# Performance work log

Hardware: AMD Instinct MI355X
Metric: run time of the kernel (lower is better)

## Reference

```python
import jax, jax.numpy as jnp
from jax import lax
import numpy as np
import math

# --- static config (matches init_kwargs) ---
B, L, C_IN = 64, 1024, 16
D, H, D_FF = 256, 8, 1024
HS, E_LAYERS, OUT = 256, 2, 1
MA, FACTOR = 25, 3
TOP_K = int(FACTOR * math.log(L))  # 20


def _ln(x, g, b, eps=1e-5):
    m = x.mean(-1, keepdims=True)
    v = ((x - m) ** 2).mean(-1, keepdims=True)
    return (x - m) / jnp.sqrt(v + eps) * g + b


def _series_decomp(x, k):
    # x: [B, L, C]; replicate-pad then moving average (AvgPool1d stride 1)
    pad = (k - 1) // 2
    front = jnp.repeat(x[:, :1, :], pad, axis=1)
    end = jnp.repeat(x[:, -1:, :], pad, axis=1)
    xp = jnp.concatenate([front, x, end], axis=1)  # [B, L+k-1, C]
    cs = jnp.cumsum(xp, axis=1)
    cs = jnp.concatenate([jnp.zeros_like(cs[:, :1]), cs], axis=1)
    mm = (cs[:, k:] - cs[:, :-k]) / k  # [B, L, C]
    return x - mm, mm


def _autocorrelation(q, k, v):
    # q,k,v: [B, L, H, E] -> eval-mode Autoformer AutoCorrelation
    Bq, Lq, Hq, Eq = q.shape
    qf = jnp.fft.rfft(q.transpose(0, 2, 3, 1), axis=-1)  # [B,H,E,F]
    kf = jnp.fft.rfft(k.transpose(0, 2, 3, 1), axis=-1)
    corr = jnp.fft.irfft(qf * jnp.conj(kf), n=Lq, axis=-1)  # [B,H,E,L]
    mean_value = corr.mean(axis=(1, 2))  # [B, L]
    weights, delay = lax.top_k(mean_value, TOP_K)  # [B, K]
    tmp_corr = jax.nn.softmax(weights, axis=-1)
    vals = v.transpose(0, 2, 3, 1)  # [B,H,E,L]
    init = jnp.arange(Lq)

    def step(acc, dw):
        d, w = dw  # d: [B] int, w: [B] float
        idx = (init[None, :] + d[:, None]) % Lq  # circular delayed gather == roll
        pat = jnp.take_along_axis(vals, idx[:, None, None, :], axis=-1)
        return acc + pat * w[:, None, None, None], None

    agg, _ = lax.scan(step, jnp.zeros_like(vals), (delay.T, tmp_corr.T))
    return agg.transpose(0, 3, 1, 2)  # [B, L, H, E]


def _forward(x_enc, conv1_w, conv1_b, conv2_w, conv2_b, cnn_ln_g, cnn_ln_b,
             proj_w, proj_b, proj_ln_g, proj_ln_b,
             Wq, bq, Wk, bk, Wv, bv, Wo, bo, Wff1, Wff2,
             rp1_w, rp1_b, rp_ln_g, rp_ln_b, rp2_w, rp2_b):
    Bb = x_enc.shape[0]
    dn = ('NCH', 'OIH', 'NCH')
    # CNN frontend (dropout = identity in eval)
    h = lax.conv_general_dilated(x_enc.transpose(0, 2, 1), conv1_w, (1,), [(1, 1)],
                                 dimension_numbers=dn) + conv1_b[None, :, None]
    h = jax.nn.relu(h)
    h = lax.conv_general_dilated(h, conv2_w, (1,), [(1, 1)],
                                 dimension_numbers=dn) + conv2_b[None, :, None]
    h = jax.nn.relu(h)
    enc = _ln(h.transpose(0, 2, 1), cnn_ln_g, cnn_ln_b)  # [B, L, D]

    pooled_parts = []
    for i in range(E_LAYERS):
        q = (enc @ Wq[i] + bq[i]).reshape(Bb, L, H, D // H)
        k = (enc @ Wk[i] + bk[i]).reshape(Bb, L, H, D // H)
        v = (enc @ Wv[i] + bv[i]).reshape(Bb, L, H, D // H)
        ac = _autocorrelation(q, k, v).reshape(Bb, L, D)
        new_x = ac @ Wo[i] + bo[i]
        x = enc + new_x
        x, _ = _series_decomp(x, MA)
        y = jax.nn.gelu(jnp.einsum('bld,fd->blf', x, Wff1[i]), approximate=False)
        y = jnp.einsum('blf,df->bld', y, Wff2[i])
        enc, _ = _series_decomp(x + y, MA)
        pooled_parts.append(enc[:, -1, :])

    pooled = jnp.concatenate(pooled_parts, axis=-1)  # [B, e_layers*D]
    input_embed = _ln(jax.nn.relu(x_enc.reshape(Bb, -1) @ proj_w + proj_b),
                      proj_ln_g, proj_ln_b)  # [B, HS]
    final = jnp.concatenate([pooled, input_embed], axis=-1)
    o = jax.nn.relu(final @ rp1_w + rp1_b)
    o = _ln(o, rp_ln_g, rp_ln_b)
    o = o @ rp2_w + rp2_b  # [B, 1]
    return o.squeeze(-1)


def setup_inputs() -> dict:
    key = jax.random.key(0)
    ks = iter(jax.random.split(key, 32))

    def nrm(shape, s=0.02):
        return jax.random.normal(next(ks), shape, jnp.float32) * s

    inp = {
        'x_enc': jax.random.normal(next(ks), (B, L, C_IN), jnp.float32),
        'conv1_w': nrm((D, C_IN, 3), 0.1), 'conv1_b': jnp.zeros((D,), jnp.float32),
        'conv2_w': nrm((D, D, 3), 0.05), 'conv2_b': jnp.zeros((D,), jnp.float32),
        'cnn_ln_g': jnp.ones((D,), jnp.float32), 'cnn_ln_b': jnp.zeros((D,), jnp.float32),
        'proj_w': nrm((L * C_IN, HS)), 'proj_b': jnp.zeros((HS,), jnp.float32),
        'proj_ln_g': jnp.ones((HS,), jnp.float32), 'proj_ln_b': jnp.zeros((HS,), jnp.float32),
        'Wq': nrm((E_LAYERS, D, D)), 'bq': jnp.zeros((E_LAYERS, D), jnp.float32),
        'Wk': nrm((E_LAYERS, D, D)), 'bk': jnp.zeros((E_LAYERS, D), jnp.float32),
        'Wv': nrm((E_LAYERS, D, D)), 'bv': jnp.zeros((E_LAYERS, D), jnp.float32),
        'Wo': nrm((E_LAYERS, D, D)), 'bo': jnp.zeros((E_LAYERS, D), jnp.float32),
        'Wff1': nrm((E_LAYERS, D_FF, D)),
        'Wff2': nrm((E_LAYERS, D, D_FF)),
        'rp1_w': nrm((E_LAYERS * D + HS, HS)), 'rp1_b': jnp.zeros((HS,), jnp.float32),
        'rp_ln_g': jnp.ones((HS,), jnp.float32), 'rp_ln_b': jnp.zeros((HS,), jnp.float32),
        'rp2_w': nrm((HS, OUT)), 'rp2_b': jnp.zeros((OUT,), jnp.float32),
    }
    return inp


def reference(x_enc, conv1_w, conv1_b, conv2_w, conv2_b, cnn_ln_g, cnn_ln_b,
              proj_w, proj_b, proj_ln_g, proj_ln_b,
              Wq, bq, Wk, bk, Wv, bv, Wo, bo, Wff1, Wff2,
              rp1_w, rp1_b, rp_ln_g, rp_ln_b, rp2_w, rp2_b):
    return _forward(x_enc, conv1_w, conv1_b, conv2_w, conv2_b, cnn_ln_g, cnn_ln_b,
                    proj_w, proj_b, proj_ln_g, proj_ln_b,
                    Wq, bq, Wk, bk, Wv, bv, Wo, bo, Wff1, Wff2,
                    rp1_w, rp1_b, rp_ln_g, rp_ln_b, rp2_w, rp2_b)
```

## Files before the change

### kernel.cpp

```cpp
#include <hip/hip_runtime.h>
#include <math.h>

#define FLAG_ACC     1
#define FLAG_RELU    2
#define FLAG_GELU    4
#define FLAG_ABF16   8
#define FLAG_OBF16  16
#define FLAG_RESB16 32

typedef __attribute__((ext_vector_type(8))) short short8;
typedef __attribute__((ext_vector_type(4))) short short4v;
typedef __attribute__((ext_vector_type(4))) float f32x4;

__device__ __forceinline__ short f2bf(float f) {
  unsigned u = __builtin_bit_cast(unsigned, f);
  unsigned r = u + 0x7fffu + ((u >> 16) & 1u);
  return (short)(r >> 16);
}
__device__ __forceinline__ float bf2f(short s) {
  unsigned u = ((unsigned)(unsigned short)s) << 16;
  return __builtin_bit_cast(float, u);
}
__device__ __forceinline__ void load_lds16(const void* g, void* lds) {
  __builtin_amdgcn_global_load_lds(
      (const __attribute__((address_space(1))) void*)g,
      (__attribute__((address_space(3))) void*)lds, 16, 0, 0);
}

__global__ __launch_bounds__(256) void gemm_f32(
    const float* __restrict__ A, const float* __restrict__ B, float* __restrict__ C,
    int M, int N, int K, int a_shift,
    const float* __restrict__ bias, const float* __restrict__ residual, int flags)
{
  __shared__ float As[16][65];
  __shared__ float Bs[16][64];
  const int tid = threadIdx.x;
  const int tx = tid & 15, ty = tid >> 4;
  const int row0 = blockIdx.y * 64;
  const int col0 = blockIdx.x * 64;
  int kbeg = 0, kend = K;
  if ((int)gridDim.z > 1) {
    int kchunk = ((K + (int)gridDim.z - 1) / (int)gridDim.z + 15) & ~15;
    kbeg = (int)blockIdx.z * kchunk;
    kend = min(K, kbeg + kchunk);
  }
  float acc[4][4] = {};
  const int a_m = tid >> 2;
  const int a_k = (tid & 3) << 2;
  const int b_n = (tid & 15) << 2;
  const int b_k = tid >> 4;
  for (int k0 = kbeg; k0 < kend; k0 += 16) {
    int srow = row0 + a_m + a_shift;
    float4 av = make_float4(0.f, 0.f, 0.f, 0.f);
    if (srow >= 0 && srow < M)
      av = *reinterpret_cast<const float4*>(A + (long long)srow * K + (k0 + a_k));
    As[a_k + 0][a_m] = av.x; As[a_k + 1][a_m] = av.y;
    As[a_k + 2][a_m] = av.z; As[a_k + 3][a_m] = av.w;
    float4 bv = make_float4(0.f, 0.f, 0.f, 0.f);
    int brow = k0 + b_k;
    if (brow < K)
      bv = *reinterpret_cast<const float4*>(B + (long long)brow * N + (col0 + b_n));
    Bs[b_k][b_n + 0] = bv.x; Bs[b_k][b_n + 1] = bv.y;
    Bs[b_k][b_n + 2] = bv.z; Bs[b_k][b_n + 3] = bv.w;
    __syncthreads();
#pragma unroll
    for (int kk = 0; kk < 16; kk++) {
      float ar[4], br[4];
#pragma unroll
      for (int i = 0; i < 4; i++) ar[i] = As[kk][ty * 4 + i];
#pragma unroll
      for (int j = 0; j < 4; j++) br[j] = Bs[kk][tx * 4 + j];
#pragma unroll
      for (int i = 0; i < 4; i++)
#pragma unroll
        for (int j = 0; j < 4; j++)
          acc[i][j] += ar[i] * br[j];
    }
    __syncthreads();
  }
  if ((int)gridDim.z > 1) {
#pragma unroll
    for (int i = 0; i < 4; i++) {
      int r = row0 + ty * 4 + i; if (r >= M) continue;
#pragma unroll
      for (int j = 0; j < 4; j++) {
        int c = col0 + tx * 4 + j; if (c >= N) continue;
        atomicAdd(&C[(long long)r * N + c], acc[i][j]);
      }
    }
    return;
  }
#pragma unroll
  for (int i = 0; i < 4; i++) {
    int r = row0 + ty * 4 + i; if (r >= M) continue;
#pragma unroll
    for (int j = 0; j < 4; j++) {
      int c = col0 + tx * 4 + j; if (c >= N) continue;
      float v = acc[i][j];
      if (bias)     v += bias[c];
      if (residual) v += residual[(long long)r * N + c];
      if (flags & FLAG_ACC)  v += C[(long long)r * N + c];
      if (flags & FLAG_RELU) v = fmaxf(v, 0.f);
      if (flags & FLAG_GELU) v = 0.5f * v * (1.f + erff(v * 0.70710678118654752f));
      C[(long long)r * N + c] = v;
    }
  }
}

__global__ __launch_bounds__(512) void gemm_bt8(
    const void* __restrict__ Av, const short* __restrict__ Btb, void* __restrict__ Cv,
    const float* __restrict__ residual, const float* __restrict__ bias,
    int M, int N, int K, int lda, int flags, int tapped)
{
  __shared__ __align__(16) short Asl[8192];
  __shared__ __align__(16) short Bsl[8192];
  const int tid = threadIdx.x;
  const int row0 = blockIdx.x * 128;
  const int col0 = blockIdx.y * 128;
  const int lane = tid & 63;
  const int wave = tid >> 6;
  const int wm = (wave >> 1) * 32;
  const int wn = (wave & 1) * 64;
  const int fm = lane & 15;
  const int k8c = lane >> 4;
  const int mr = tid >> 2;
  const int mkc = tid & 3;
  const int msw = mr & 7;
  const bool a_dma = (flags & FLAG_ABF16) && !tapped;

  f32x4 acc[2][4] = {};
  for (int k0 = 0; k0 < K; k0 += 64) {
    __syncthreads();
#pragma unroll
    for (int u = 0; u < 2; u++) {
      int p = (wave * 2 + u) * 64 + lane;
      int r = p >> 3;
      int kc = (p & 7) ^ (r & 7);
      load_lds16(Btb + (long long)(col0 + r) * K + k0 + kc * 8,
                 (char*)Bsl + (wave * 2 + u) * 1024);
    }
    if (a_dma) {
      const short* Ab = (const short*)Av;
#pragma unroll
      for (int u = 0; u < 2; u++) {
        int p = (wave * 2 + u) * 64 + lane;
        int r = p >> 3;
        int kc = (p & 7) ^ (r & 7);
        load_lds16(Ab + (long long)(row0 + r) * lda + k0 + kc * 8,
                   (char*)Asl + (wave * 2 + u) * 1024);
      }
    } else {
      int arow = row0 + mr + (tapped ? (k0 >> 8) - 1 : 0);
      int acol = tapped ? (k0 & 255) : k0;
      bool ok = (arow >= 0 && arow < M);
      if (flags & FLAG_ABF16) {
        const short* ga = (const short*)Av + (long long)arow * lda + acol + mkc * 16;
        short8 z;
#pragma unroll
        for (int u = 0; u < 8; u++) z[u] = 0;
#pragma unroll
        for (int j = 0; j < 2; j++) {
          short8 v = ok ? *(const short8*)(ga + j * 8) : z;
          *(short8*)&Asl[(mr * 8 + ((mkc * 2 + j) ^ msw)) * 8] = v;
        }
      } else {
        const float* ga = (const float*)Av + (long long)arow * lda + acol + mkc * 16;
#pragma unroll
        for (int j = 0; j < 2; j++) {
          float4 f0 = make_float4(0.f,0.f,0.f,0.f), f1 = f0;
          if (ok) { f0 = *(const float4*)(ga + j * 8); f1 = *(const float4*)(ga + j * 8 + 4); }
          short8 v;
          v[0]=f2bf(f0.x); v[1]=f2bf(f0.y); v[2]=f2bf(f0.z); v[3]=f2bf(f0.w);
          v[4]=f2bf(f1.x); v[5]=f2bf(f1.y); v[6]=f2bf(f1.z); v[7]=f2bf(f1.w);
          *(short8*)&Asl[(mr * 8 + ((mkc * 2 + j) ^ msw)) * 8] = v;
        }
      }
    }
    __syncthreads();
#pragma unroll
    for (int kk8 = 0; kk8 < 8; kk8 += 4) {
      short8 af[2], bf[4];
#pragma unroll
      for (int i = 0; i < 2; i++) {
        int r = wm + i * 16 + fm;
        af[i] = *(short8*)&Asl[(r * 8 + ((kk8 + k8c) ^ (r & 7))) * 8];
      }
#pragma unroll
      for (int j = 0; j < 4; j++) {
        int r = wn + j * 16 + fm;
        bf[j] = *(short8*)&Bsl[(r * 8 + ((kk8 + k8c) ^ (r & 7))) * 8];
      }
#pragma unroll
      for (int i = 0; i < 2; i++)
#pragma unroll
        for (int j = 0; j < 4; j++)
          acc[i][j] = __builtin_amdgcn_mfma_f32_16x16x32_bf16(af[i], bf[j], acc[i][j], 0, 0, 0);
    }
  }
#pragma unroll
  for (int i = 0; i < 2; i++) {
    const int mbase = row0 + wm + i * 16 + (lane >> 4) * 4;
#pragma unroll
    for (int j = 0; j < 4; j++) {
      const int n = col0 + wn + j * 16 + fm;
      const float bs = bias ? bias[n] : 0.f;
#pragma unroll
      for (int r = 0; r < 4; r++) {
        long long idx = (long long)(mbase + r) * N + n;
        float v = acc[i][j][r] + bs;
        if (residual) {
          if (flags & FLAG_RESB16) v += bf2f(((const short*)residual)[idx]);
          else                     v += residual[idx];
        }
        if (flags & FLAG_ACC)  v += ((const float*)Cv)[idx];
        if (flags & FLAG_RELU) v = fmaxf(v, 0.f);
        if (flags & FLAG_GELU) v = 0.5f * v * (1.f + erff(v * 0.70710678118654752f));
        if (flags & FLAG_OBF16) ((short*)Cv)[idx] = f2bf(v);
        else                    ((float*)Cv)[idx] = v;
      }
    }
  }
}

__global__ __launch_bounds__(512) void gemm_qkT(
    const short* __restrict__ Ab, const short* __restrict__ Bth,
    const short* __restrict__ Btl, float* __restrict__ QT,
    const float* __restrict__ bias, int K)
{
  __shared__ __align__(16) char smem[24576];
  short* Asl = (short*)smem;
  short* Bhi = (short*)(smem + 8192);
  short* Blo = (short*)(smem + 16384);
  const int tid = threadIdx.x;
  const int row0 = blockIdx.x * 128;
  const int col0 = blockIdx.y * 128;
  const int lane = tid & 63;
  const int wave = tid >> 6;
  const int wm = (wave >> 1) * 32;
  const int wn = (wave & 1) * 64;
  const int fm = lane & 15;
  const int k8c = lane >> 4;

  f32x4 acc[2][4] = {};
  for (int k0 = 0; k0 < K; k0 += 32) {
    __syncthreads();
    {
      int p = wave * 64 + lane;
      int r = p >> 2;
      int kc = (p & 3) ^ ((r >> 1) & 3);
      long long ao = (long long)(row0 + r) * 256 + k0 + kc * 8;
      long long go = (long long)(col0 + r) * K + k0 + kc * 8;
      int lo = wave * 1024;
      load_lds16(Ab + ao, (char*)Asl + lo);
      load_lds16(Bth + go, (char*)Bhi + lo);
      load_lds16(Btl + go, (char*)Blo + lo);
    }
    __syncthreads();
    short8 af[2], bh[4], bl[4];
#pragma unroll
    for (int i = 0; i < 2; i++) {
      int r = wm + i * 16 + fm;
      af[i] = *(short8*)&Asl[(r * 4 + (k8c ^ ((r >> 1) & 3))) * 8];
    }
#pragma unroll
    for (int j = 0; j < 4; j++) {
      int r = wn + j * 16 + fm;
      int p = (r * 4 + (k8c ^ ((r >> 1) & 3))) * 8;
      bh[j] = *(short8*)&Bhi[p];
      bl[j] = *(short8*)&Blo[p];
    }
#pragma unroll
    for (int i = 0; i < 2; i++)
#pragma unroll
      for (int j = 0; j < 4; j++) {
        acc[i][j] = __builtin_amdgcn_mfma_f32_16x16x32_bf16(af[i], bh[j], acc[i][j], 0, 0, 0);
        acc[i][j] = __builtin_amdgcn_mfma_f32_16x16x32_bf16(af[i], bl[j], acc[i][j], 0, 0, 0);
      }
  }
#pragma unroll
  for (int i = 0; i < 2; i++) {
    const int mbase = row0 + wm + i * 16 + (lane >> 4) * 4;
    const int bb = mbase >> 10;
    const int l  = mbase & 1023;
#pragma unroll
    for (int j = 0; j < 4; j++) {
      const int n = col0 + wn + j * 16 + fm;
      const float bs = bias[n];
      float4 o = make_float4(acc[i][j][0] + bs, acc[i][j][1] + bs,
                             acc[i][j][2] + bs, acc[i][j][3] + bs);
      *(float4*)&QT[((long long)(bb * 512 + n) << 10) + l] = o;
    }
  }
}

#define SKW(i) ((i) + ((i) >> 5))

__device__ __forceinline__ int rev4_10(int f) {
  return ((f & 3) << 8) | (((f >> 2) & 3) << 6) | (((f >> 4) & 3) << 4)
       | (((f >> 6) & 3) << 2) | ((f >> 8) & 3);
}

template<int M, bool INV, int NCH>
__device__ __forceinline__ void fft_stageN(float2 (*__restrict__ buf)[1056],
                                           const float2* __restrict__ tw, int t) {
  constexpr int LOG2M = (M == 256) ? 8 : (M == 64) ? 6 : (M == 16) ? 4 : (M == 4) ? 2 : 0;
  const int j = t & (M - 1);
  const int base = ((t >> LOG2M) << (LOG2M + 2)) | j;
  float2 w = tw[SKW(j << (8 - LOG2M))];
  const float c1 = w.x, s1 = INV ? -w.y : w.y;
  const float c2 = c1 * c1 - s1 * s1, s2 = 2.f * c1 * s1;
  const float c3 = c2 * c1 - s2 * s1, s3 = c2 * s1 + s2 * c1;
#pragma unroll
  for (int ch = 0; ch < NCH; ch++) {
    float2* s = buf[ch];
    float2 a0 = s[SKW(base)];
    float2 b0 = s[SKW(base + M)];
    float2 d0 = s[SKW(base + 2 * M)];
    float2 e0 = s[SKW(base + 3 * M)];
    float t0r = a0.x + d0.x, t0i = a0.y + d0.y;
    float t1r = a0.x - d0.x, t1i = a0.y - d0.y;
    float t2r = b0.x + e0.x, t2i = b0.y + e0.y;
    float t3r = b0.x - e0.x, t3i = b0.y - e0.y;
    float y0r = t0r + t2r, y0i = t0i + t2i;
    float y2r = t0r - t2r, y2i = t0i - t2i;
    float y1r, y1i, y3r, y3i;
    if (!INV) { y1r = t1r + t3i; y1i = t1i - t3r; y3r = t1r - t3i; y3i = t1i + t3r; }
    else      { y1r = t1r - t3i; y1i = t1i + t3r; y3r = t1r + t3i; y3i = t1i - t3r; }
    s[SKW(base)]         = make_float2(y0r, y0i);
    s[SKW(base + M)]     = make_float2(y1r * c1 - y1i * s1, y1r * s1 + y1i * c1);
    s[SKW(base + 2 * M)] = make_float2(y2r * c2 - y2i * s2, y2r * s2 + y2i * c2);
    s[SKW(base + 3 * M)] = make_float2(y3r * c3 - y3i * s3, y3r * s3 + y3i * c3);
  }
}

__global__ __launch_bounds__(256) void fft_cross(
    const float* __restrict__ QT, float* __restrict__ Rpart)
{
  __shared__ float2 buf[4][1056];
  __shared__ float2 tw[264];
  const int tid = threadIdx.x;
  const int b = blockIdx.x & 63;
  const int g = blockIdx.x >> 6;
  {
    float s, c;
    sincosf(-1.5707963267948966f * (float)tid * (1.f / 256.f), &s, &c);
    tw[SKW(tid)] = make_float2(c, s);
  }
  const float* Qb = QT + (long long)b * 524288;
  const int c0 = g * 16;
  float4 qv[4], kv[4];
#pragma unroll
  for (int c = 0; c < 4; c++) {
    qv[c] = *(const float4*)(Qb + ((long long)(c0 + c) << 10) + tid * 4);
    kv[c] = *(const float4*)(Qb + ((long long)(256 + c0 + c) << 10) + tid * 4);
  }
  float aR[4] = {0.f, 0.f, 0.f, 0.f}, aI[4] = {0.f, 0.f, 0.f, 0.f};
  __syncthreads();
  for (int q4 = 0; q4 < 4; q4++) {
    const int i0 = tid * 4;
#pragma unroll
    for (int c = 0; c < 4; c++) {
      buf[c][SKW(i0 + 0)] = make_float2(qv[c].x, kv[c].x);
      buf[c][SKW(i0 + 1)] = make_float2(qv[c].y, kv[c].y);
      buf[c][SKW(i0 + 2)] = make_float2(qv[c].z, kv[c].z);
      buf[c][SKW(i0 + 3)] = make_float2(qv[c].w, kv[c].w);
    }
    if (q4 < 3) {
      const int cb = c0 + (q4 + 1) * 4;
#pragma unroll
      for (int c = 0; c < 4; c++) {
        qv[c] = *(const float4*)(Qb + ((long long)(cb + c) << 10) + tid * 4);
        kv[c] = *(const float4*)(Qb + ((long long)(256 + cb + c) << 10) + tid * 4);
      }
    }
    __syncthreads();
    fft_stageN<256, false, 4>(buf, tw, tid); __syncthreads();
    fft_stageN<64,  false, 4>(buf, tw, tid); __syncthreads();
    fft_stageN<16,  false, 4>(buf, tw, tid); __syncthreads();
    fft_stageN<4,   false, 4>(buf, tw, tid); __syncthreads();
    fft_stageN<1,   false, 4>(buf, tw, tid); __syncthreads();
#pragma unroll
    for (int u = 0; u < 4; u++) {
      const int f = tid + (u << 8);
      const int p1 = SKW(rev4_10(f));
      const int p2 = SKW(rev4_10((1024 - f) & 1023));
#pragma unroll
      for (int c = 0; c < 4; c++) {
        float2 z1 = buf[c][p1];
        float2 z2 = buf[c][p2];
        float Qr = 0.5f * (z1.x + z2.x), Qi = 0.5f * (z1.y - z2.y);
        float Kr = 0.5f * (z1.y + z2.y), Ki = 0.5f * (z2.x - z1.x);
        aR[u] += Qr * Kr + Qi * Ki;
        aI[u] += Qi * Kr - Qr * Ki;
      }
    }
    __syncthreads();
  }
  float* Rp = Rpart + (long long)(g * 64 + b) * 2048;
#pragma unroll
  for (int u = 0; u < 4; u++) {
    Rp[tid + (u << 8)] = aR[u];
    Rp[1024 + tid + (u << 8)] = aI[u];
  }
}

__global__ __launch_bounds__(256) void fft_inv(
    const float* __restrict__ Rpart, float* __restrict__ MV)
{
  __shared__ float2 ping[1056], tw[264];
  const int tid = threadIdx.x;
  const int b = blockIdx.x;
  {
    float s, c;
    sincosf(-1.5707963267948966f * (float)tid * (1.f / 256.f), &s, &c);
    tw[SKW(tid)] = make_float2(c, s);
  }
#pragma unroll
  for (int u = 0; u < 4; u++) {
    int f = tid + (u << 8);
    float sr = 0.f, si = 0.f;
#pragma unroll
    for (int g = 0; g < 16; g++) {
      const float* Rp = Rpart + (long long)(g * 64 + b) * 2048;
      sr += Rp[f];
      si += Rp[1024 + f];
    }
    ping[SKW(f)] = make_float2(sr, si);
  }
  __syncthreads();
  float2 (*bp)[1056] = reinterpret_cast<float2 (*)[1056]>(ping);
  fft_stageN<256, true, 1>(bp, tw, tid); __syncthreads();
  fft_stageN<64,  true, 1>(bp, tw, tid); __syncthreads();
  fft_stageN<16,  true, 1>(bp, tw, tid); __syncthreads();
  fft_stageN<4,   true, 1>(bp, tw, tid); __syncthreads();
  fft_stageN<1,   true, 1>(bp, tw, tid); __syncthreads();
  const float sc = 1.f / (1024.f * 256.f);
#pragma unroll
  for (int u = 0; u < 4; u++) {
    int p = tid + (u << 8);
    MV[(long long)b * 1024 + rev4_10(p)] = ping[SKW(p)].x * sc;
  }
}

__global__ void prep_weights(
    const float* __restrict__ conv2_w, const float* __restrict__ Wq,
    const float* __restrict__ Wk, const float* __restrict__ Wff1,
    const float* __restrict__ Wff2,
    const float* __restrict__ bq, const float* __restrict__ bk,
    short* __restrict__ CB2Tb, short* __restrict__ QKTH, short* __restrict__ QKTL,
    short* __restrict__ WFF1b, short* __restrict__ WFF2b, float* __restrict__ BQK)
{
  const int total = 196608 + 262144 + 524288 + 524288 + 1024;
  for (int idx = blockIdx.x * 256 + threadIdx.x; idx < total;
       idx += gridDim.x * 256) {
    int t = idx;
    if (t < 196608) {
      int o = t / 768, rem = t % 768, kk = rem >> 8, i = rem & 255;
      CB2Tb[t] = f2bf(conv2_w[(o * 256 + i) * 3 + kk]);
    } else if ((t -= 196608) < 262144) {
      int L = t >> 17, rem = t & 131071, r = rem >> 8, k = rem & 255;
      float val = (r < 256) ? Wq[L * 65536 + k * 256 + r]
                            : Wk[L * 65536 + k * 256 + (r - 256)];
      short h = f2bf(val);
      QKTH[t] = h;
      QKTL[t] = f2bf(val - bf2f(h));
    } else if ((t -= 262144) < 524288) {
      WFF1b[t] = f2bf(Wff1[t]);
    } else if ((t -= 524288) < 524288) {
      WFF2b[t] = f2bf(Wff2[t]);
    } else {
      t -= 524288;
      int L = t >> 9, j = t & 511;
      BQK[t] = (j < 256) ? bq[L * 256 + j] : bk[L * 256 + (j - 256)];
    }
  }
}

__global__ void vo_finish(const float* __restrict__ WVO, const float* __restrict__ Wo,
                          const float* __restrict__ bv, const float* __restrict__ bo,
                          short* __restrict__ WVOTb, float* __restrict__ BVO)
{
  const int total = 131072 + 512;
  for (int idx = blockIdx.x * 256 + threadIdx.x; idx < total;
       idx += gridDim.x * 256) {
    if (idx < 131072) {
      int L = idx >> 16, rem = idx & 65535, n = rem >> 8, k = rem & 255;
      WVOTb[idx] = f2bf(WVO[L * 65536 + k * 256 + n]);
    } else {
      int j = idx - 131072;
      int L = j >> 8, n = j & 255;
      float acc = bo[L * 256 + n];
      for (int k = 0; k < 256; k++)
        acc += bv[L * 256 + k] * Wo[(long long)L * 65536 + k * 256 + n];
      BVO[j] = acc;
    }
  }
}

__global__ __launch_bounds__(256) void conv1_direct(
    const float* __restrict__ x, const float* __restrict__ w,
    const float* __restrict__ bias, short* __restrict__ out)
{
  __shared__ float xs[66][16];
  const int b = blockIdx.y, lg = blockIdx.x, tid = threadIdx.x;
  const int l0 = lg * 64;
  for (int idx = tid; idx < 1056; idx += 256) {
    int r = idx >> 4, c = idx & 15;
    int l = l0 + r - 1;
    xs[r][c] = (l >= 0 && l < 1024) ? x[((long long)b * 1024 + l) * 16 + c] : 0.f;
  }
  float wr[48];
#pragma unroll
  for (int u = 0; u < 48; u++) wr[u] = w[tid * 48 + u];
  const float bs = bias[tid];
  __syncthreads();
  for (int r = 0; r < 64; r++) {
    float acc = bs;
#pragma unroll
    for (int i = 0; i < 16; i++) {
      acc += xs[r + 0][i] * wr[i * 3 + 0];
      acc += xs[r + 1][i] * wr[i * 3 + 1];
      acc += xs[r + 2][i] * wr[i * 3 + 2];
    }
    out[((long long)b * 1024 + l0 + r) * 256 + tid] = f2bf(fmaxf(acc, 0.f));
  }
}

__global__ __launch_bounds__(256) void fixup_conv_b(
    short* __restrict__ h, const short* __restrict__ src,
    const short* __restrict__ w2b, const float* __restrict__ bias)
{
  __shared__ __align__(16) short srows[512];
  const int b = blockIdx.x >> 1;
  const int edge = blockIdx.x & 1;
  const int l = edge ? 1023 : 0;
  const int o = threadIdx.x;
  const int t0 = edge ? 1022 : 0;
  const int kk0 = edge ? 0 : 1;
  if (threadIdx.x < 64) {
    int rr = threadIdx.x >> 5, cc = threadIdx.x & 31;
    ((short8*)srows)[rr * 32 + cc] =
        ((const short8*)(src + ((long long)b * 1024 + t0 + rr) * 256))[cc];
  }
  __syncthreads();
  float acc = bias[o];
  const short* w0 = w2b + o * 768 + kk0 * 256;
  const short* w1 = w0 + 256;
#pragma unroll
  for (int c8 = 0; c8 < 32; c8++) {
    short8 wv0 = *(const short8*)(w0 + c8 * 8);
    short8 wv1 = *(const short8*)(w1 + c8 * 8);
    short8 x0 = ((short8*)srows)[c8];
    short8 x1 = ((short8*)srows)[32 + c8];
#pragma unroll
    for (int j = 0; j < 8; j++)
      acc += bf2f(x0[j]) * bf2f(wv0[j]) + bf2f(x1[j]) * bf2f(wv1[j]);
  }
  h[((long long)b * 1024 + l) * 256 + o] = f2bf(fmaxf(acc, 0.f));
}

__global__ __launch_bounds__(256) void ln_rows4(
    const float* __restrict__ in, float* __restrict__ out,
    const float* __restrict__ g, const float* __restrict__ b,
    int prerelu, int out_stride, int out_off)
{
  const int row = blockIdx.x * 4 + (threadIdx.x >> 6);
  const int lane = threadIdx.x & 63;
  float4 x = ((const float4*)(in + (long long)row * 256))[lane];
  if (prerelu) {
    x.x = fmaxf(x.x, 0.f); x.y = fmaxf(x.y, 0.f);
    x.z = fmaxf(x.z, 0.f); x.w = fmaxf(x.w, 0.f);
  }
  float s = x.x + x.y + x.z + x.w;
#pragma unroll
  for (int o = 32; o > 0; o >>= 1) s += __shfl_xor(s, o, 64);
  float mean = s * (1.f / 256.f);
  float4 d = make_float4(x.x - mean, x.y - mean, x.z - mean, x.w - mean);
  float s2 = d.x * d.x + d.y * d.y + d.z * d.z + d.w * d.w;
#pragma unroll
  for (int o = 32; o > 0; o >>= 1) s2 += __shfl_xor(s2, o, 64);
  float rsd = rsqrtf(s2 * (1.f / 256.f) + 1e-5f);
  float4 gg = ((const float4*)g)[lane];
  float4 bb = ((const float4*)b)[lane];
  float4 o4 = make_float4(d.x * rsd * gg.x + bb.x, d.y * rsd * gg.y + bb.y,
                          d.z * rsd * gg.z + bb.z, d.w * rsd * gg.w + bb.w);
  ((float4*)(out + (long long)row * out_stride + out_off))[lane] = o4;
}

__global__ __launch_bounds__(256) void ln_rows4bb(
    const short* __restrict__ in, short* __restrict__ out,
    const float* __restrict__ g, const float* __restrict__ b)
{
  const int row = blockIdx.x * 4 + (threadIdx.x >> 6);
  const int lane = threadIdx.x & 63;
  short4v xb = ((const short4v*)in)[(long long)row * 64 + lane];
  float4 x = make_float4(bf2f(xb[0]), bf2f(xb[1]), bf2f(xb[2]), bf2f(xb[3]));
  float s = x.x + x.y + x.z + x.w;
#pragma unroll
  for (int o = 32; o > 0; o >>= 1) s += __shfl_xor(s, o, 64);
  float mean = s * (1.f / 256.f);
  float4 d = make_float4(x.x - mean, x.y - mean, x.z - mean, x.w - mean);
  float s2 = d.x * d.x + d.y * d.y + d.z * d.z + d.w * d.w;
#pragma unroll
  for (int o = 32; o > 0; o >>= 1) s2 += __shfl_xor(s2, o, 64);
  float rsd = rsqrtf(s2 * (1.f / 256.f) + 1e-5f);
  float4 gg = ((const float4*)g)[lane];
  float4 bb = ((const float4*)b)[lane];
  short4v o4;
  o4[0] = f2bf(d.x * rsd * gg.x + bb.x);
  o4[1] = f2bf(d.y * rsd * gg.y + bb.y);
  o4[2] = f2bf(d.z * rsd * gg.z + bb.z);
  o4[3] = f2bf(d.w * rsd * gg.w + bb.w);
  ((short4v*)out)[(long long)row * 64 + lane] = o4;
}

__global__ void decomp4bf(const short* __restrict__ in, short* __restrict__ out,
                          float* __restrict__ fin, int finoff)
{
  const int id = blockIdx.x;
  const int c = id & 7;
  const int s = id >> 3;
  const int b = c + 8 * (s >> 8);
  const int lg = s & 255;
  const int l = lg * 4 + (threadIdx.x >> 6);
  const int c4 = threadIdx.x & 63;
  const short4v* base = (const short4v*)(in + (long long)b * 262144);
  float4 acc = make_float4(0.f, 0.f, 0.f, 0.f);
#pragma unroll
  for (int j = -12; j <= 12; j++) {
    int t = l + j;
    t = t < 0 ? 0 : (t > 1023 ? 1023 : t);
    short4v x = base[t * 64 + c4];
    acc.x += bf2f(x[0]); acc.y += bf2f(x[1]);
    acc.z += bf2f(x[2]); acc.w += bf2f(x[3]);
  }
  short4v x0 = base[l * 64 + c4];
  float4 o = make_float4(bf2f(x0[0]) - acc.x * (1.f / 25.f),
                         bf2f(x0[1]) - acc.y * (1.f / 25.f),
                         bf2f(x0[2]) - acc.z * (1.f / 25.f),
                         bf2f(x0[3]) - acc.w * (1.f / 25.f));
  short4v ob;
  ob[0] = f2bf(o.x); ob[1] = f2bf(o.y); ob[2] = f2bf(o.z); ob[3] = f2bf(o.w);
  ((short4v*)out)[((long long)b * 1024 + l) * 64 + c4] = ob;
  if (l == 1023) {
    float* f = fin + (long long)b * 768 + finoff + c4 * 4;
    f[0] = o.x; f[1] = o.y; f[2] = o.z; f[3] = o.w;
  }
}

__global__ void decomp4b(const short* __restrict__ in, short* __restrict__ out)
{
  const int id = blockIdx.x;
  const int c = id & 7;
  const int s = id >> 3;
  const int b = c + 8 * (s >> 8);
  const int lg = s & 255;
  const int l = lg * 4 + (threadIdx.x >> 6);
  const int c4 = threadIdx.x & 63;
  const short4v* base = (const short4v*)(in + (long long)b * 262144);
  float4 acc = make_float4(0.f, 0.f, 0.f, 0.f);
#pragma unroll
  for (int j = -12; j <= 12; j++) {
    int t = l + j;
    t = t < 0 ? 0 : (t > 1023 ? 1023 : t);
    short4v x = base[t * 64 + c4];
    acc.x += bf2f(x[0]); acc.y += bf2f(x[1]);
    acc.z += bf2f(x[2]); acc.w += bf2f(x[3]);
  }
  short4v x0 = base[l * 64 + c4];
  short4v o;
  o[0] = f2bf(bf2f(x0[0]) - acc.x * (1.f / 25.f));
  o[1] = f2bf(bf2f(x0[1]) - acc.y * (1.f / 25.f));
  o[2] = f2bf(bf2f(x0[2]) - acc.z * (1.f / 25.f));
  o[3] = f2bf(bf2f(x0[3]) - acc.w * (1.f / 25.f));
  ((short4v*)(out + (long long)b * 262144))[l * 64 + c4] = o;
}

__global__ __launch_bounds__(64) void topk_softmax_wave(
    const float* __restrict__ mv, float* __restrict__ wts, int* __restrict__ dly)
{
  const int b = blockIdx.x, lane = threadIdx.x;
  float v[16];
#pragma unroll
  for (int j = 0; j < 16; j++)
    v[j] = mv[(long long)b * 1024 + lane + 64 * j];
  float selv = 0.f; int seli = 0;
  for (int it = 0; it < 20; it++) {
    float bv = -1e30f; int bi = 0x7fffffff;
#pragma unroll
    for (int j = 0; j < 16; j++) {
      float x = v[j]; int idx = lane + 64 * j;
      if (x > bv || (x == bv && idx < bi)) { bv = x; bi = idx; }
    }
#pragma unroll
    for (int off = 32; off > 0; off >>= 1) {
      float ov = __shfl_xor(bv, off, 64);
      int   oi = __shfl_xor(bi, off, 64);
      if (ov > bv || (ov == bv && oi < bi)) { bv = ov; bi = oi; }
    }
    if (lane == it) { selv = bv; seli = bi; }
    if ((bi & 63) == lane) v[bi >> 6] = -1e30f;
  }
  const float w0 = __shfl(selv, 0, 64);
  float e = (lane < 20) ? __expf(selv - w0) : 0.f;
  float s = e;
#pragma unroll
  for (int off = 32; off > 0; off >>= 1) s += __shfl_xor(s, off, 64);
  if (lane < 20) {
    wts[b * 20 + lane] = e / s;
    dly[b * 20 + lane] = seli;
  }
}

__global__ void agg4b(const short* __restrict__ enc, const float* __restrict__ wts,
                      const int* __restrict__ dly, short* __restrict__ out)
{
  const int id = blockIdx.x;
  const int c = id & 7;
  const int s = id >> 3;
  const int b = c + 8 * (s >> 8);
  const int lg = s & 255;
  const int l = lg * 4 + (threadIdx.x >> 6);
  const int c4 = threadIdx.x & 63;
  const short4v* vb = (const short4v*)(enc + (long long)b * 262144);
  float4 acc = make_float4(0.f, 0.f, 0.f, 0.f);
  for (int kk = 0; kk < 20; kk++) {
    int d = dly[b * 20 + kk];
    float w = wts[b * 20 + kk];
    short4v x = vb[((l + d) & 1023) * 64 + c4];
    acc.x += w * bf2f(x[0]); acc.y += w * bf2f(x[1]);
    acc.z += w * bf2f(x[2]); acc.w += w * bf2f(x[3]);
  }
  short4v o;
  o[0] = f2bf(acc.x); o[1] = f2bf(acc.y); o[2] = f2bf(acc.z); o[3] = f2bf(acc.w);
  ((short4v*)(out + (long long)b * 262144))[l * 64 + c4] = o;
}

__global__ void init_bias(float* __restrict__ C, const float* __restrict__ bias)
{
  C[(long long)blockIdx.x * 256 + threadIdx.x] = bias[threadIdx.x];
}

__global__ void rp2_kernel(const float* __restrict__ x, const float* __restrict__ w,
// ... 148 lines not shown
```

Before: 1.278 ms.

## Stage QK GEMM epilogue through LDS and split FFT buffers into planar arrays

The QK projection epilogue now transposes its accumulator tile through shared memory in four column chunks, so each thread writes contiguous 32-byte runs of the transposed QT output instead of scattered float4 stores. Separately, the FFT kernels switch from interleaved float2 shared buffers to split real and imaginary float arrays, with matching split twiddle tables. The planar layout is meant to reduce LDS bank conflicts in the radix-4 stages. The epilogue adds extra barriers and reuses the GEMM shared memory, which assumes that region is large enough.

Result: slower. 1.331 ms (+4.1%).

```diff
diff --git a/kernel.cpp b/kernel.cpp
--- a/kernel.cpp
+++ b/kernel.cpp
@@ -277,19 +277,35 @@
         acc[i][j] = __builtin_amdgcn_mfma_f32_16x16x32_bf16(af[i], bl[j], acc[i][j], 0, 0, 0);
       }
   }
-#pragma unroll
-  for (int i = 0; i < 2; i++) {
-    const int mbase = row0 + wm + i * 16 + (lane >> 4) * 4;
-    const int bb = mbase >> 10;
-    const int l  = mbase & 1023;
-#pragma unroll
-    for (int j = 0; j < 4; j++) {
-      const int n = col0 + wn + j * 16 + fm;
-      const float bs = bias[n];
-      float4 o = make_float4(acc[i][j][0] + bs, acc[i][j][1] + bs,
-                             acc[i][j][2] + bs, acc[i][j][3] + bs);
-      *(float4*)&QT[((long long)(bb * 512 + n) << 10) + l] = o;
-    }
+  float* Tt = (float*)smem;
+  const int bb = row0 >> 10;
+  const int lbase = row0 & 1023;
+#pragma unroll
+  for (int ch = 0; ch < 4; ch++) {
+    __syncthreads();
+    int rel = ch * 32 - wn;
+    if (rel >= 0 && rel < 64) {
+      int j0 = rel >> 4;
+#pragma unroll
+      for (int jj = 0; jj < 2; jj++) {
+        int j = j0 + jj;
+        int nl = j * 16 + fm - rel;
+        float bs = bias[col0 + wn + j * 16 + fm];
+#pragma unroll
+        for (int i = 0; i < 2; i++) {
+          int l = wm + i * 16 + (lane >> 4) * 4;
+          *(float4*)&Tt[nl * 132 + l] = make_float4(
+              acc[i][j][0] + bs, acc[i][j][1] + bs,
+              acc[i][j][2] + bs, acc[i][j][3] + bs);
+        }
+      }
+    }
+    __syncthreads();
+    int col = tid >> 4;
+    int l0 = (tid & 15) * 8;
+    long long base = (((long long)(bb * 512 + col0 + ch * 32 + col)) << 10) + lbase + l0;
+    *(float4*)&QT[base]     = *(float4*)&Tt[col * 132 + l0];
+    *(float4*)&QT[base + 4] = *(float4*)&Tt[col * 132 + l0 + 4];
   }
 }
 
@@ -301,50 +317,54 @@
 }
 
 template<int M, bool INV, int NCH>
-__device__ __forceinline__ void fft_stageN(float2 (*__restrict__ buf)[1056],
-                                           const float2* __restrict__ tw, int t) {
+__device__ __forceinline__ void fft_stageS(float (*__restrict__ re)[1056],
+                                           float (*__restrict__ im)[1056],
+                                           const float* __restrict__ twc,
+                                           const float* __restrict__ tws, int t) {
   constexpr int LOG2M = (M == 256) ? 8 : (M == 64) ? 6 : (M == 16) ? 4 : (M == 4) ? 2 : 0;
   const int j = t & (M - 1);
   const int base = ((t >> LOG2M) << (LOG2M + 2)) | j;
-  float2 w = tw[SKW(j << (8 - LOG2M))];
-  const float c1 = w.x, s1 = INV ? -w.y : w.y;
+  const int ti = SKW(j << (8 - LOG2M));
+  const float c1 = twc[ti];
+  const float s1 = INV ? -tws[ti] : tws[ti];
   const float c2 = c1 * c1 - s1 * s1, s2 = 2.f * c1 * s1;
   const float c3 = c2 * c1 - s2 * s1, s3 = c2 * s1 + s2 * c1;
+  const int p0 = SKW(base), p1 = SKW(base + M), p2 = SKW(base + 2 * M), p3 = SKW(base + 3 * M);
 #pragma unroll
   for (int ch = 0; ch < NCH; ch++) {
-    float2* s = buf[ch];
-    float2 a0 = s[SKW(base)];
-    float2 b0 = s[SKW(base + M)];
-    float2 d0 = s[SKW(base + 2 * M)];
-    float2 e0 = s[SKW(base + 3 * M)];
-    float t0r = a0.x + d0.x, t0i = a0.y + d0.y;
-    float t1r = a0.x - d0.x, t1i = a0.y - d0.y;
-    float t2r = b0.x + e0.x, t2i = b0.y + e0.y;
-    float t3r = b0.x - e0.x, t3i = b0.y - e0.y;
+    float a0r = re[ch][p0], a0i = im[ch][p0];
+    float b0r = re[ch][p1], b0i = im[ch][p1];
+    float d0r = re[ch][p2], d0i = im[ch][p2];
+    float e0r = re[ch][p3], e0i = im[ch][p3];
+    float t0r = a0r + d0r, t0i = a0i + d0i;
+    float t1r = a0r - d0r, t1i = a0i - d0i;
+    float t2r = b0r + e0r, t2i = b0i + e0i;
+    float t3r = b0r - e0r, t3i = b0i - e0i;
     float y0r = t0r + t2r, y0i = t0i + t2i;
     float y2r = t0r - t2r, y2i = t0i - t2i;
     float y1r, y1i, y3r, y3i;
     if (!INV) { y1r = t1r + t3i; y1i = t1i - t3r; y3r = t1r - t3i; y3i = t1i + t3r; }
     else      { y1r = t1r - t3i; y1i = t1i + t3r; y3r = t1r + t3i; y3i = t1i - t3r; }
-    s[SKW(base)]         = make_float2(y0r, y0i);
-    s[SKW(base + M)]     = make_float2(y1r * c1 - y1i * s1, y1r * s1 + y1i * c1);
-    s[SKW(base + 2 * M)] = make_float2(y2r * c2 - y2i * s2, y2r * s2 + y2i * c2);
-    s[SKW(base + 3 * M)] = make_float2(y3r * c3 - y3i * s3, y3r * s3 + y3i * c3);
+    re[ch][p0] = y0r;                       im[ch][p0] = y0i;
+    re[ch][p1] = y1r * c1 - y1i * s1;       im[ch][p1] = y1r * s1 + y1i * c1;
+    re[ch][p2] = y2r * c2 - y2i * s2;       im[ch][p2] = y2r * s2 + y2i * c2;
+    re[ch][p3] = y3r * c3 - y3i * s3;       im[ch][p3] = y3r * s3 + y3i * c3;
   }
 }
 
 __global__ __launch_bounds__(256) void fft_cross(
     const float* __restrict__ QT, float* __restrict__ Rpart)
 {
-  __shared__ float2 buf[4][1056];
-  __shared__ float2 tw[264];
+  __shared__ float bre[4][1056], bim[4][1056];
+  __shared__ float twc[264], tws[264];
   const int tid = threadIdx.x;
   const int b = blockIdx.x & 63;
   const int g = blockIdx.x >> 6;
   {
     float s, c;
     sincosf(-1.5707963267948966f * (float)tid * (1.f / 256.f), &s, &c);
-    tw[SKW(tid)] = make_float2(c, s);
+    twc[SKW(tid)] = c;
+    tws[SKW(tid)] = s;
   }
   const float* Qb = QT + (long long)b * 524288;
   const int c0 = g * 16;
@@ -360,10 +380,10 @@
     const int i0 = tid * 4;
 #pragma unroll
     for (int c = 0; c < 4; c++) {
-      buf[c][SKW(i0 + 0)] = make_float2(qv[c].x, kv[c].x);
-      buf[c][SKW(i0 + 1)] = make_float2(qv[c].y, kv[c].y);
-      buf[c][SKW(i0 + 2)] = make_float2(qv[c].z, kv[c].z);
-      buf[c][SKW(i0 + 3)] = make_float2(qv[c].w, kv[c].w);
+      bre[c][SKW(i0 + 0)] = qv[c].x;  bim[c][SKW(i0 + 0)] = kv[c].x;
+      bre[c][SKW(i0 + 1)] = qv[c].y;  bim[c][SKW(i0 + 1)] = kv[c].y;
+      bre[c][SKW(i0 + 2)] = qv[c].z;  bim[c][SKW(i0 + 2)] = kv[c].z;
+      bre[c][SKW(i0 + 3)] = qv[c].w;  bim[c][SKW(i0 + 3)] = kv[c].w;
     }
     if (q4 < 3) {
       const int cb = c0 + (q4 + 1) * 4;
@@ -374,11 +394,11 @@
       }
     }
     __syncthreads();
-    fft_stageN<256, false, 4>(buf, tw, tid); __syncthreads();
-    fft_stageN<64,  false, 4>(buf, tw, tid); __syncthreads();
-    fft_stageN<16,  false, 4>(buf, tw, tid); __syncthreads();
-    fft_stageN<4,   false, 4>(buf, tw, tid); __syncthreads();
-    fft_stageN<1,   false, 4>(buf, tw, tid); __syncthreads();
+    fft_stageS<256, false, 4>(bre, bim, twc, tws, tid); __syncthreads();
+    fft_stageS<64,  false, 4>(bre, bim, twc, tws, tid); __syncthreads();
+    fft_stageS<16,  false, 4>(bre, bim, twc, tws, tid); __syncthreads();
+    fft_stageS<4,   false, 4>(bre, bim, twc, tws, tid); __syncthreads();
+    fft_stageS<1,   false, 4>(bre, bim, twc, tws, tid); __syncthreads();
 #pragma unroll
     for (int u = 0; u < 4; u++) {
       const int f = tid + (u << 8);
@@ -386,10 +406,10 @@
       const int p2 = SKW(rev4_10((1024 - f) & 1023));
 #pragma unroll
       for (int c = 0; c < 4; c++) {
-        float2 z1 = buf[c][p1];
-        float2 z2 = buf[c][p2];
-        float Qr = 0.5f * (z1.x + z2.x), Qi = 0.5f * (z1.y - z2.y);
-        float Kr = 0.5f * (z1.y + z2.y), Ki = 0.5f * (z2.x - z1.x);
+        float z1r = bre[c][p1], z1i = bim[c][p1];
+        float z2r = bre[c][p2], z2i = bim[c][p2];
+        float Qr = 0.5f * (z1r + z2r), Qi = 0.5f * (z1i - z2i);
+        float Kr = 0.5f * (z1i + z2i), Ki = 0.5f * (z2r - z1r);
         aR[u] += Qr * Kr + Qi * Ki;
         aI[u] += Qi * Kr - Qr * Ki;
       }
@@ -407,13 +427,15 @@
 __global__ __launch_bounds__(256) void fft_inv(
     const float* __restrict__ Rpart, float* __restrict__ MV)
 {
-  __shared__ float2 ping[1056], tw[264];
+  __shared__ float pre[1][1056], pim[1][1056];
+  __shared__ float twc[264], tws[264];
   const int tid = threadIdx.x;
   const int b = blockIdx.x;
   {
     float s, c;
     sincosf(-1.5707963267948966f * (float)tid * (1.f / 256.f), &s, &c);
-    tw[SKW(tid)] = make_float2(c, s);
+    twc[SKW(tid)] = c;
+    tws[SKW(tid)] = s;
   }
 #pragma unroll
   for (int u = 0; u < 4; u++) {
@@ -425,20 +447,20 @@
       sr += Rp[f];
       si += Rp[1024 + f];
     }
-    ping[SKW(f)] = make_float2(sr, si);
+    pre[0][SKW(f)] = sr;
+    pim[0][SKW(f)] = si;
   }
   __syncthreads();
-  float2 (*bp)[1056] = reinterpret_cast<float2 (*)[1056]>(ping);
-  fft_stageN<256, true, 1>(bp, tw, tid); __syncthreads();
-  fft_stageN<64,  true, 1>(bp, tw, tid); __syncthreads();
-  fft_stageN<16,  true, 1>(bp, tw, tid); __syncthreads();
-  fft_stageN<4,   true, 1>(bp, tw, tid); __syncthreads();
-  fft_stageN<1,   true, 1>(bp, tw, tid); __syncthreads();
+  fft_stageS<256, true, 1>(pre, pim, twc, tws, tid); __syncthreads();
+  fft_stageS<64,  true, 1>(pre, pim, twc, tws, tid); __syncthreads();
+  fft_stageS<16,  true, 1>(pre, pim, twc, tws, tid); __syncthreads();
+  fft_stageS<4,   true, 1>(pre, pim, twc, tws, tid); __syncthreads();
+  fft_stageS<1,   true, 1>(pre, pim, twc, tws, tid); __syncthreads();
   const float sc = 1.f / (1024.f * 256.f);
 #pragma unroll
   for (int u = 0; u < 4; u++) {
     int p = tid + (u << 8);
-    MV[(long long)b * 1024 + rev4_10(p)] = ping[SKW(p)].x * sc;
+    MV[(long long)b * 1024 + rev4_10(p)] = pre[0][SKW(p)] * sc;
   }
 }
 
```

## Fuse forward FFT radix-4 stages into register-resident radix-16 passes

Applied to the files above, without the earlier changes.

The forward FFT in fft_cross is reorganised so that each 64-thread group owns one channel and performs two radix-4 stages per pass in registers (16 elements per thread). This cuts the five LDS round trips and barriers to three. The inverse FFT keeps the old per-stage code under a renamed single-channel helper. Holding 16 complex values per thread raises register pressure, and the new strided LDS access patterns may hit bank conflicts.

Result: slower. 1.323 ms (+3.5%).

```diff
diff --git a/kernel.cpp b/kernel.cpp
--- a/kernel.cpp
+++ b/kernel.cpp
@@ -300,37 +300,32 @@
        | (((f >> 6) & 3) << 2) | ((f >> 8) & 3);
 }
 
-template<int M, bool INV, int NCH>
-__device__ __forceinline__ void fft_stageN(float2 (*__restrict__ buf)[1056],
-                                           const float2* __restrict__ tw, int t) {
-  constexpr int LOG2M = (M == 256) ? 8 : (M == 64) ? 6 : (M == 16) ? 4 : (M == 4) ? 2 : 0;
-  const int j = t & (M - 1);
-  const int base = ((t >> LOG2M) << (LOG2M + 2)) | j;
-  float2 w = tw[SKW(j << (8 - LOG2M))];
-  const float c1 = w.x, s1 = INV ? -w.y : w.y;
-  const float c2 = c1 * c1 - s1 * s1, s2 = 2.f * c1 * s1;
-  const float c3 = c2 * c1 - s2 * s1, s3 = c2 * s1 + s2 * c1;
-#pragma unroll
-  for (int ch = 0; ch < NCH; ch++) {
-    float2* s = buf[ch];
-    float2 a0 = s[SKW(base)];
-    float2 b0 = s[SKW(base + M)];
-    float2 d0 = s[SKW(base + 2 * M)];
-    float2 e0 = s[SKW(base + 3 * M)];
-    float t0r = a0.x + d0.x, t0i = a0.y + d0.y;
-    float t1r = a0.x - d0.x, t1i = a0.y - d0.y;
-    float t2r = b0.x + e0.x, t2i = b0.y + e0.y;
-    float t3r = b0.x - e0.x, t3i = b0.y - e0.y;
-    float y0r = t0r + t2r, y0i = t0i + t2i;
-    float y2r = t0r - t2r, y2i = t0i - t2i;
-    float y1r, y1i, y3r, y3i;
-    if (!INV) { y1r = t1r + t3i; y1i = t1i - t3r; y3r = t1r - t3i; y3i = t1i + t3r; }
-    else      { y1r = t1r - t3i; y1i = t1i + t3r; y3r = t1r + t3i; y3i = t1i - t3r; }
-    s[SKW(base)]         = make_float2(y0r, y0i);
-    s[SKW(base + M)]     = make_float2(y1r * c1 - y1i * s1, y1r * s1 + y1i * c1);
-    s[SKW(base + 2 * M)] = make_float2(y2r * c2 - y2i * s2, y2r * s2 + y2i * c2);
-    s[SKW(base + 3 * M)] = make_float2(y3r * c3 - y3i * s3, y3r * s3 + y3i * c3);
-  }
+__device__ __forceinline__ void bfly4(float2& A, float2& B, float2& C, float2& D,
+                                      float c1, float s1) {
+  float t0r = A.x + C.x, t0i = A.y + C.y;
+  float t1r = A.x - C.x, t1i = A.y - C.y;
+  float t2r = B.x + D.x, t2i = B.y + D.y;
+  float t3r = B.x - D.x, t3i = B.y - D.y;
+  float y0r = t0r + t2r, y0i = t0i + t2i;
+  float y2r = t0r - t2r, y2i = t0i - t2i;
+  float y1r = t1r + t3i, y1i = t1i - t3r;
+  float y3r = t1r - t3i, y3i = t1i + t3r;
+  float c2 = c1 * c1 - s1 * s1, s2 = 2.f * c1 * s1;
+  float c3 = c2 * c1 - s2 * s1, s3 = c2 * s1 + s2 * c1;
+  A = make_float2(y0r, y0i);
+  B = make_float2(y1r * c1 - y1i * s1, y1r * s1 + y1i * c1);
+  C = make_float2(y2r * c2 - y2i * s2, y2r * s2 + y2i * c2);
+  D = make_float2(y3r * c3 - y3i * s3, y3r * s3 + y3i * c3);
+}
+__device__ __forceinline__ void bfly4_nw(float2& A, float2& B, float2& C, float2& D) {
+  float t0r = A.x + C.x, t0i = A.y + C.y;
+  float t1r = A.x - C.x, t1i = A.y - C.y;
+  float t2r = B.x + D.x, t2i = B.y + D.y;
+  float t3r = B.x - D.x, t3i = B.y - D.y;
+  A = make_float2(t0r + t2r, t0i + t2i);
+  C = make_float2(t0r - t2r, t0i - t2i);
+  B = make_float2(t1r + t3i, t1i - t3r);
+  D = make_float2(t1r - t3i, t1i + t3r);
 }
 
 __global__ __launch_bounds__(256) void fft_cross(
@@ -348,6 +343,9 @@
   }
   const float* Qb = QT + (long long)b * 524288;
   const int c0 = g * 16;
+  const int ch = tid >> 6;
+  const int sl = tid & 63;
+  float2* S = buf[ch];
   float4 qv[4], kv[4];
 #pragma unroll
   for (int c = 0; c < 4; c++) {
@@ -374,11 +372,70 @@
       }
     }
     __syncthreads();
-    fft_stageN<256, false, 4>(buf, tw, tid); __syncthreads();
-    fft_stageN<64,  false, 4>(buf, tw, tid); __syncthreads();
-    fft_stageN<16,  false, 4>(buf, tw, tid); __syncthreads();
-    fft_stageN<4,   false, 4>(buf, tw, tid); __syncthreads();
-    fft_stageN<1,   false, 4>(buf, tw, tid); __syncthreads();
+    {
+      float2 e[4][4];
+#pragma unroll
+      for (int bb = 0; bb < 4; bb++)
+#pragma unroll
+        for (int a = 0; a < 4; a++)
+          e[bb][a] = S[SKW(sl + a * 64 + bb * 256)];
+#pragma unroll
+      for (int a = 0; a < 4; a++) {
+        float2 w = tw[SKW(sl + a * 64)];
+        bfly4(e[0][a], e[1][a], e[2][a], e[3][a], w.x, w.y);
+      }
+      {
+        float2 w = tw[SKW(sl << 2)];
+#pragma unroll
+        for (int bb = 0; bb < 4; bb++)
+          bfly4(e[bb][0], e[bb][1], e[bb][2], e[bb][3], w.x, w.y);
+      }
+#pragma unroll
+      for (int bb = 0; bb < 4; bb++)
+#pragma unroll
+        for (int a = 0; a < 4; a++)
+          S[SKW(sl + a * 64 + bb * 256)] = e[bb][a];
+    }
+    __syncthreads();
+    {
+      const int blk = (sl >> 2) * 64;
+      const int r = sl & 3;
+      float2 f2[4][4];
+#pragma unroll
+      for (int cc = 0; cc < 4; cc++)
+#pragma unroll
+        for (int a = 0; a < 4; a++)
+          f2[cc][a] = S[SKW(blk + cc * 16 + a * 4 + r)];
+#pragma unroll
+      for (int a = 0; a < 4; a++) {
+        float2 w = tw[SKW((r + a * 4) << 4)];
+        bfly4(f2[0][a], f2[1][a], f2[2][a], f2[3][a], w.x, w.y);
+      }
+      {
+        float2 w = tw[SKW(r << 6)];
+#pragma unroll
+        for (int cc = 0; cc < 4; cc++)
+          bfly4(f2[cc][0], f2[cc][1], f2[cc][2], f2[cc][3], w.x, w.y);
+      }
+#pragma unroll
+      for (int cc = 0; cc < 4; cc++)
+#pragma unroll
+        for (int a = 0; a < 4; a++)
+          S[SKW(blk + cc * 16 + a * 4 + r)] = f2[cc][a];
+    }
+    __syncthreads();
+    {
+#pragma unroll
+      for (int q = 0; q < 4; q++) {
+        int p0 = sl * 16 + q * 4;
+        float2 A = S[SKW(p0)], B = S[SKW(p0 + 1)];
+        float2 C = S[SKW(p0 + 2)], D = S[SKW(p0 + 3)];
+        bfly4_nw(A, B, C, D);
+        S[SKW(p0)] = A; S[SKW(p0 + 1)] = B;
+        S[SKW(p0 + 2)] = C; S[SKW(p0 + 3)] = D;
+      }
+    }
+    __syncthreads();
 #pragma unroll
     for (int u = 0; u < 4; u++) {
       const int f = tid + (u << 8);
@@ -404,6 +461,35 @@
   }
 }
 
+template<int M, bool INV>
+__device__ __forceinline__ void fft_stage1(float2* __restrict__ s,
+                                           const float2* __restrict__ tw, int t) {
+  constexpr int LOG2M = (M == 256) ? 8 : (M == 64) ? 6 : (M == 16) ? 4 : (M == 4) ? 2 : 0;
+  const int j = t & (M - 1);
+  const int base = ((t >> LOG2M) << (LOG2M + 2)) | j;
+  float2 w = tw[SKW(j << (8 - LOG2M))];
+  const float c1 = w.x, s1 = INV ? -w.y : w.y;
+  const float c2 = c1 * c1 - s1 * s1, s2 = 2.f * c1 * s1;
+  const float c3 = c2 * c1 - s2 * s1, s3 = c2 * s1 + s2 * c1;
+  float2 a0 = s[SKW(base)];
+  float2 b0 = s[SKW(base + M)];
+  float2 d0 = s[SKW(base + 2 * M)];
+  float2 e0 = s[SKW(base + 3 * M)];
+  float t0r = a0.x + d0.x, t0i = a0.y + d0.y;
+  float t1r = a0.x - d0.x, t1i = a0.y - d0.y;
+  float t2r = b0.x + e0.x, t2i = b0.y + e0.y;
+  float t3r = b0.x - e0.x, t3i = b0.y - e0.y;
+  float y0r = t0r + t2r, y0i = t0i + t2i;
+  float y2r = t0r - t2r, y2i = t0i - t2i;
+  float y1r, y1i, y3r, y3i;
+  if (!INV) { y1r = t1r + t3i; y1i = t1i - t3r; y3r = t1r - t3i; y3i = t1i + t3r; }
+  else      { y1r = t1r - t3i; y1i = t1i + t3r; y3r = t1r + t3i; y3i = t1i - t3r; }
+  s[SKW(base)]         = make_float2(y0r, y0i);
+  s[SKW(base + M)]     = make_float2(y1r * c1 - y1i * s1, y1r * s1 + y1i * c1);
+  s[SKW(base + 2 * M)] = make_float2(y2r * c2 - y2i * s2, y2r * s2 + y2i * c2);
+  s[SKW(base + 3 * M)] = make_float2(y3r * c3 - y3i * s3, y3r * s3 + y3i * c3);
+}
+
 __global__ __launch_bounds__(256) void fft_inv(
     const float* __restrict__ Rpart, float* __restrict__ MV)
 {
@@ -428,12 +514,11 @@
     ping[SKW(f)] = make_float2(sr, si);
   }
   __syncthreads();
-  float2 (*bp)[1056] = reinterpret_cast<float2 (*)[1056]>(ping);
-  fft_stageN<256, true, 1>(bp, tw, tid); __syncthreads();
-  fft_stageN<64,  true, 1>(bp, tw, tid); __syncthreads();
-  fft_stageN<16,  true, 1>(bp, tw, tid); __syncthreads();
-  fft_stageN<4,   true, 1>(bp, tw, tid); __syncthreads();
-  fft_stageN<1,   true, 1>(bp, tw, tid); __syncthreads();
+  fft_stage1<256, true>(ping, tw, tid); __syncthreads();
+  fft_stage1<64,  true>(ping, tw, tid); __syncthreads();
+  fft_stage1<16,  true>(ping, tw, tid); __syncthreads();
+  fft_stage1<4,   true>(ping, tw, tid); __syncthreads();
+  fft_stage1<1,   true>(ping, tw, tid); __syncthreads();
   const float sc = 1.f / (1024.f * 256.f);
 #pragma unroll
   for (int u = 0; u < 4; u++) {
```
